# Kernel tuning notes

Hardware: AMD Instinct MI355X
Metric: run time of the kernel (lower is better)

The kernel has to match this reference:

```python
import jax, jax.numpy as jnp
import numpy as np
from jax import lax

B, C, H, W = 2, 3, 112, 112
PERCENTILE = 95.0


def setup_inputs() -> dict:
    key = jax.random.key(0)
    kx, ky = jax.random.split(key)
    x = jax.random.normal(kx, (B, C, H, W), dtype=jnp.float32)
    y = jax.random.randint(ky, (B, H, W), 0, C)
    return {"x": x, "y": y}


def _masked_quantile(vals, mask, q):
    # torch.quantile (linear interpolation) over entries of `vals` where mask is True.
    n = jnp.sum(mask)
    s = jnp.sort(jnp.where(mask, vals, jnp.inf))  # valid entries first, inf-padded
    pos = q * jnp.maximum(n - 1, 0).astype(vals.dtype)
    lo = jnp.floor(pos).astype(jnp.int32)
    hi = jnp.ceil(pos).astype(jnp.int32)
    frac = pos - lo.astype(vals.dtype)
    v = s[lo] * (1.0 - frac) + s[hi] * frac
    return jnp.where(n > 0, v, jnp.zeros((), vals.dtype))


def _forward(x, y):
    b, c = x.shape[0], x.shape[1]
    n = H * W
    pred = jnp.argmax(x, axis=1).reshape(b, n)   # [b, N] predicted labels
    gt = y.reshape(b, n).astype(pred.dtype)      # [b, N] gt labels

    # voxel coordinates of the full grid; nonzero() point sets become boolean masks over it
    ii, jj = jnp.meshgrid(jnp.arange(H, dtype=jnp.float32),
                          jnp.arange(W, dtype=jnp.float32), indexing="ij")
    coords = jnp.stack([ii.ravel(), jj.ravel()], axis=1)  # [N, 2]
    sq = jnp.sum(coords * coords, axis=1)
    d2 = sq[:, None] + sq[None, :] - 2.0 * (coords @ coords.T)
    D = jnp.sqrt(jnp.maximum(d2, 0.0))  # [N, N] symmetric all-pairs voxel distances

    cls = jnp.arange(c, dtype=pred.dtype)
    seg_masks = (pred[:, None, :] == cls[None, :, None]).reshape(b * c, n)  # [b*c, N]
    gt_masks = (gt[:, None, :] == cls[None, :, None]).reshape(b * c, n)
    q = jnp.float32(PERCENTILE / 100.0)

    def one(masks):
        seg_m, gt_m = masks
        # min distance from every voxel to the gt / seg point set
        d_to_gt = jnp.min(jnp.where(gt_m[None, :], D, jnp.inf), axis=1)   # [N]
        d_to_seg = jnp.min(jnp.where(seg_m[None, :], D, jnp.inf), axis=1)  # [N]
        hd1 = _masked_quantile(d_to_gt, seg_m, q)   # over seg points
        hd2 = _masked_quantile(d_to_seg, gt_m, q)   # over gt points
        hd = jnp.maximum(hd1, hd2)
        ok = (jnp.sum(seg_m) > 0) & (jnp.sum(gt_m) > 0)  # empty set -> 0.0
        return jnp.where(ok, hd, jnp.zeros((), D.dtype))

    hd_vals = lax.map(one, (seg_masks, gt_masks))  # sequential over b*c pairs, one [N,N] temp at a time
    return jnp.mean(hd_vals)


def reference(x, y):
    return _forward(x, y)
```

## Files before the change

### kernel.cpp

```cpp
#include <hip/hip_runtime.h>

#define BB 2
#define CC 3
#define HH 112
#define WW 112
#define NN (HH*WW)
#define NPAIR (BB*CC)
#define NCOMBO (NPAIR*2)
#define NBINS 24643
#define HWORDS ((NBINS+1)/2)
#define INF29 (1<<29)
#define RCH 8
#define NCHUNK (HH/RCH)
#define NTHR 1024
#define NFW (NN/64)
#define POISON 0xAAAAAAAAu
#define CSTRIDE 16
#define CTR_INTS ((NCOMBO+1)*CSTRIDE)

typedef unsigned long long ull;

__device__ __forceinline__ int predLab(const float* __restrict__ xb) {
    float v0 = xb[0], v1 = xb[NN], v2 = xb[2*(size_t)NN];
    int lab = 0; float best = v0;
    if (v1 > best) { best = v1; lab = 1; }
    if (v2 > best) lab = 2;
    return lab;
}

__device__ __forceinline__ void sinku(unsigned v) { asm volatile("" :: "v"(v)); }
__device__ __forceinline__ void sinkf(float v)    { asm volatile("" :: "v"(v)); }

union Smem {
    struct {
        ull flatW[NFW];
        unsigned colQ[4][WW];
        int G[RCH][WW];
    } ab;
    unsigned hist[HWORDS];
};

__global__ __launch_bounds__(NTHR) void fused_kernel(
        const float* __restrict__ x, const int* __restrict__ yl,
        unsigned* __restrict__ ghist, unsigned* __restrict__ ctrs,
        float* __restrict__ qvalg, int* __restrict__ qcntg,
        float* __restrict__ out) {
    __shared__ Smem sm;
    __shared__ int pscan[NTHR];
    __shared__ float vlh[2];
    __shared__ int lastFlag, gLastFlag;

    const int tid = threadIdx.x;
    const int m     = blockIdx.x / NCHUNK;
    const int chunk = blockIdx.x % NCHUNK;
    const int r0 = chunk * RCH;
    const int pair = m >> 1, src = m & 1;
    const int b = pair / CC, c = pair % CC;
    const float* xb = x + (size_t)b * CC * NN;
    const int*   yb = yl + b * NN;
    unsigned* ghm = ghist + m * HWORDS;
    unsigned* ctr = ctrs + m * CSTRIDE;

    const int lane = tid & 63, wid = tid >> 6;
    #pragma unroll
    for (int k = 0; k < (NN + NTHR - 1)/NTHR; k++) {
        int v = k*NTHR + tid;
        bool in = (v < NN);
        int lab = 0;
        if (in) lab = src ? predLab(xb + v) : yb[v];
        ull m64 = __ballot(in && lab == c);
        int w = k*(NTHR/64) + wid;
        if (lane == 0 && w < NFW) sm.ab.flatW[w] = m64;
    }
    __syncthreads();

    if (tid < 4*WW) {
        int xcolT = tid % WW, q = tid / WW;
        const unsigned* flatU = (const unsigned*)sm.ab.flatW;
        int jmax = (q == 3) ? (HH - 96) : 32;
        unsigned acc = 0;
        int p = (q*32)*WW + xcolT;
        for (int j = 0; j < jmax; j++) {
            acc |= ((flatU[p >> 5] >> (p & 31)) & 1u) << j;
            p += WW;
        }
        sm.ab.colQ[q][xcolT] = acc;
    }
    __syncthreads();

    const int xcol = tid % WW, rsel = tid / WW;
    const bool act = (tid < RCH*WW);

    if (act) {
        ull lo = sm.ab.colQ[0][xcol] | ((ull)sm.ab.colQ[1][xcol] << 32);
        ull hi = sm.ab.colQ[2][xcol] | ((ull)sm.ab.colQ[3][xcol] << 32);
        int r = r0 + rsel;
        ull mleLo, mleHi, mgeLo, mgeHi;
        if (r < 64) {
            mleLo = (2ull << r) - 1;  mleHi = 0;
            mgeLo = ~((1ull << r) - 1); mgeHi = ~0ull;
        } else {
            int rr = r - 64;
            mleLo = ~0ull; mleHi = (2ull << rr) - 1;
            mgeLo = 0;     mgeHi = ~((1ull << rr) - 1);
        }
        ull sL = lo & mleLo, sH = hi & mleHi;
        ull tL = lo & mgeLo, tH = hi & mgeHi;
        int posUp = sH ? (127 - (int)__builtin_clzll(sH))
                       : (sL ? (63 - (int)__builtin_clzll(sL)) : -4000);
        int posDn = tL ? (int)__builtin_ctzll(tL)
                       : (tH ? 64 + (int)__builtin_ctzll(tH) : 8000);
        int d = min(r - posUp, posDn - r);
        sm.ab.G[rsel][xcol] = d * d;
    }
    __syncthreads();

    int dreg = INF29;
    if (act) {
        int a0 = INF29, a1 = INF29, a2 = INF29, a3 = INF29;
        #pragma unroll 4
        for (int xx = 0; xx < WW; xx += 4) {
            int d0 = xcol-xx, d1 = xcol-xx-1, d2v = xcol-xx-2, d3 = xcol-xx-3;
            a0 = min(a0, d0*d0   + sm.ab.G[rsel][xx]);
            a1 = min(a1, d1*d1   + sm.ab.G[rsel][xx+1]);
            a2 = min(a2, d2v*d2v + sm.ab.G[rsel][xx+2]);
            a3 = min(a3, d3*d3   + sm.ab.G[rsel][xx+3]);
        }
        dreg = min(min(a0,a1), min(a2,a3));
    }
    __syncthreads();

    for (int i = tid; i < HWORDS; i += NTHR) sm.hist[i] = 0;
    __syncthreads();
    if (act) {
        int v = (r0 + rsel) * WW + xcol;
        int qlab = src ? yb[v] : predLab(xb + v);
        if (qlab == c) {
            int d2 = min(dreg, NBINS-1);
            atomicAdd(&sm.hist[d2 >> 1], 1u << ((d2 & 1) << 4));
        }
    }
    __syncthreads();

    for (int i = tid; i < HWORDS; i += NTHR) {
        unsigned w = sm.hist[i];
        if (w) {
            sinku(atomicCAS(&ghm[i], POISON, 0u));
            sinku(atomicAdd(&ghm[i], w));
        }
    }
    __syncthreads();

    if (tid == 0) {
        sinku(atomicCAS(ctr, POISON, 0u));
        unsigned prev = atomicAdd(ctr, 1u);
        lastFlag = (prev == NCHUNK - 1);
    }
    __syncthreads();
    if (!lastFlag) return;
    if (tid == 0) atomicExch(ctr, 0u);

    for (int i = tid; i < HWORDS; i += NTHR) {
        unsigned old = atomicExch(&ghm[i], 0u);
        if (old == POISON) old = 0u;
        sm.hist[i] = old;
    }
    __syncthreads();

    const int CHUNKB = (NBINS + NTHR - 1) / NTHR;
    int lo = tid * CHUNKB, hiE = min(lo + CHUNKB, NBINS);
    int s = 0;
    for (int i = lo; i < hiE; i++) s += (sm.hist[i >> 1] >> ((i & 1) << 4)) & 0xffff;
    pscan[tid] = s;
    __syncthreads();
    for (int off = 1; off < NTHR; off <<= 1) {
        int v = pscan[tid];
        int add = (tid >= off) ? pscan[tid - off] : 0;
        __syncthreads();
        pscan[tid] = v + add;
        __syncthreads();
    }
    int n = pscan[NTHR - 1];
    float qv = 0.f;
    if (n > 0) {
        float pos  = 0.95f * (float)(n - 1);
        int   klo  = (int)floorf(pos);
        int   khi  = (int)ceilf(pos);
        float frac = pos - (float)klo;
        int excl = pscan[tid] - s;
        for (int which = 0; which < 2; which++) {
            int r = which ? khi : klo;
            if (r >= excl && r < pscan[tid]) {
                int cacc = excl;
                for (int i = lo; i < hiE; i++) {
                    cacc += (sm.hist[i >> 1] >> ((i & 1) << 4)) & 0xffff;
                    if (cacc > r) { vlh[which] = sqrtf((float)i); break; }
                }
            }
            __syncthreads();
        }
        qv = vlh[0] * (1.f - frac) + vlh[1] * frac;
    }

    if (tid == 0) {
        sinkf(atomicExch(&qvalg[m], qv));
        sinku((unsigned)atomicExch(&qcntg[m], n));
    }
    __syncthreads();
    if (tid == 0) {
        unsigned* done = ctrs + NCOMBO * CSTRIDE;
        sinku(atomicCAS(done, POISON, 0u));
        unsigned prev = atomicAdd(done, 1u);
        gLastFlag = (prev == NCOMBO - 1);
    }
    __syncthreads();
    if (!gLastFlag) return;
    if (tid == 0) atomicExch(ctrs + NCOMBO * CSTRIDE, 0u);

    __shared__ float rq[NCOMBO];
    __shared__ int rc[NCOMBO];
    if (tid < NCOMBO) {
        rq[tid] = atomicAdd(&qvalg[tid], 0.f);
        rc[tid] = atomicAdd(&qcntg[tid], 0);
    }
    __syncthreads();
    if (tid == 0) {
        float ssum = 0.f;
        for (int p = 0; p < NPAIR; p++) {
            float hd = 0.f;
            if (rc[2*p] > 0 && rc[2*p+1] > 0)
                hd = fmaxf(rq[2*p], rq[2*p+1]);
            ssum += hd;
        }
        out[0] = ssum / (float)NPAIR;
    }
}

extern "C" void kernel_launch(void* const* d_in, const int* in_sizes, int n_in,
                              void* d_out, int out_size, void* d_ws, size_t ws_size,
                              hipStream_t stream) {
    const float* x = (const float*)d_in[0];
    const int*   y = (const int*)d_in[1];
    float* out = (float*)d_out;

    unsigned* ws    = (unsigned*)d_ws;
    unsigned* ctrs  = ws;
    unsigned* ghist = ctrs + CTR_INTS;
    float*    qvalg = (float*)(ghist + NCOMBO*HWORDS);
    int*      qcntg = (int*)(qvalg + NCOMBO);

    fused_kernel<<<NCOMBO*NCHUNK, NTHR, 0, stream>>>(x, y, ghist, ctrs,
                                                     qvalg, qcntg, out);
}
```

Baseline: 26.59 us.

## Halve row chunks, vectorize mask build, use shuffle scan and drop poison CAS

Uses 4-row chunks with 512-thread blocks, giving more, smaller blocks. The label mask is built with float4/int4 loads and shared atomicOr instead of per-element ballots. The block prefix scan now uses wave shuffles in place of a barrier-heavy Hillis-Steele loop. Per-word poison atomicCAS calls are replaced by a sentinel word subtraction, and the count array is folded into a -1 quantile marker. More blocks means the full-image mask work is repeated more often in total, and correctness now depends on the poison-initialised workspace convention.

```diff
diff --git a/kernel.cpp b/kernel.cpp
--- a/kernel.cpp
+++ b/kernel.cpp
@@ -9,46 +9,41 @@
 #define NCOMBO (NPAIR*2)
 #define NBINS 24643
 #define HWORDS ((NBINS+1)/2)
+#define HSTRIDE (HWORDS+16)
 #define INF29 (1<<29)
-#define RCH 8
+#define RCH 4
 #define NCHUNK (HH/RCH)
-#define NTHR 1024
-#define NFW (NN/64)
+#define NTHR 512
+#define NQ4 (NN/4)
+#define NFW2 (NN/32)
 #define POISON 0xAAAAAAAAu
 #define CSTRIDE 16
 #define CTR_INTS ((NCOMBO+1)*CSTRIDE)
 
 typedef unsigned long long ull;
 
-__device__ __forceinline__ int predLab(const float* __restrict__ xb) {
-    float v0 = xb[0], v1 = xb[NN], v2 = xb[2*(size_t)NN];
-    int lab = 0; float best = v0;
-    if (v1 > best) { best = v1; lab = 1; }
-    if (v2 > best) lab = 2;
+__device__ __forceinline__ int predLab3(float a, float b, float d) {
+    int lab = 0; float best = a;
+    if (b > best) { best = b; lab = 1; }
+    if (d > best) lab = 2;
     return lab;
 }
-
 __device__ __forceinline__ void sinku(unsigned v) { asm volatile("" :: "v"(v)); }
 __device__ __forceinline__ void sinkf(float v)    { asm volatile("" :: "v"(v)); }
-
-union Smem {
-    struct {
-        ull flatW[NFW];
-        unsigned colQ[4][WW];
-        int G[RCH][WW];
-    } ab;
-    unsigned hist[HWORDS];
-};
 
 __global__ __launch_bounds__(NTHR) void fused_kernel(
         const float* __restrict__ x, const int* __restrict__ yl,
         unsigned* __restrict__ ghist, unsigned* __restrict__ ctrs,
-        float* __restrict__ qvalg, int* __restrict__ qcntg,
-        float* __restrict__ out) {
-    __shared__ Smem sm;
-    __shared__ int pscan[NTHR];
+        float* __restrict__ qvalg, float* __restrict__ out) {
+    __shared__ unsigned flatU[NFW2];
+    __shared__ unsigned colQ[4][WW];
+    __shared__ int G[RCH][WW];
+    __shared__ unsigned hist[HWORDS];
+    __shared__ int wsum[NTHR/64];
     __shared__ float vlh[2];
     __shared__ int lastFlag, gLastFlag;
+    __shared__ unsigned pbase;
+    __shared__ float rq[NCOMBO];
 
     const int tid = threadIdx.x;
     const int m     = blockIdx.x / NCHUNK;
@@ -58,42 +53,57 @@
     const int b = pair / CC, c = pair % CC;
     const float* xb = x + (size_t)b * CC * NN;
     const int*   yb = yl + b * NN;
-    unsigned* ghm = ghist + m * HWORDS;
+    unsigned* ghm = ghist + m * HSTRIDE;
     unsigned* ctr = ctrs + m * CSTRIDE;
-
-    const int lane = tid & 63, wid = tid >> 6;
+    unsigned* done = ctrs + NCOMBO * CSTRIDE;
+
+    for (int i = tid; i < NFW2; i += NTHR) flatU[i] = 0u;
+    for (int i = tid; i < HWORDS; i += NTHR) hist[i] = 0u;
+    __syncthreads();
+
     #pragma unroll
-    for (int k = 0; k < (NN + NTHR - 1)/NTHR; k++) {
-        int v = k*NTHR + tid;
-        bool in = (v < NN);
-        int lab = 0;
-        if (in) lab = src ? predLab(xb + v) : yb[v];
-        ull m64 = __ballot(in && lab == c);
-        int w = k*(NTHR/64) + wid;
-        if (lane == 0 && w < NFW) sm.ab.flatW[w] = m64;
-    }
-    __syncthreads();
-
-    if (tid < 4*WW) {
+    for (int k = 0; k < (NQ4 + NTHR - 1) / NTHR; k++) {
+        int t4 = k * NTHR + tid;
+        if (t4 < NQ4) {
+            int v4 = t4 * 4;
+            unsigned nib;
+            if (src) {
+                const float4 a  = *(const float4*)(xb + v4);
+                const float4 b4 = *(const float4*)(xb + NN + v4);
+                const float4 d4 = *(const float4*)(xb + 2 * NN + v4);
+                nib  = (unsigned)(predLab3(a.x, b4.x, d4.x) == c);
+                nib |= (unsigned)(predLab3(a.y, b4.y, d4.y) == c) << 1;
+                nib |= (unsigned)(predLab3(a.z, b4.z, d4.z) == c) << 2;
+                nib |= (unsigned)(predLab3(a.w, b4.w, d4.w) == c) << 3;
+            } else {
+                const int4 yv = *(const int4*)(yb + v4);
+                nib  = (unsigned)(yv.x == c) | ((unsigned)(yv.y == c) << 1)
+                     | ((unsigned)(yv.z == c) << 2) | ((unsigned)(yv.w == c) << 3);
+            }
+            if (nib) atomicOr(&flatU[t4 >> 3], nib << ((t4 & 7) << 2));
+        }
+    }
+    __syncthreads();
+
+    if (tid < 4 * WW) {
         int xcolT = tid % WW, q = tid / WW;
-        const unsigned* flatU = (const unsigned*)sm.ab.flatW;
         int jmax = (q == 3) ? (HH - 96) : 32;
         unsigned acc = 0;
-        int p = (q*32)*WW + xcolT;
+        int p = (q * 32) * WW + xcolT;
         for (int j = 0; j < jmax; j++) {
             acc |= ((flatU[p >> 5] >> (p & 31)) & 1u) << j;
             p += WW;
         }
-        sm.ab.colQ[q][xcolT] = acc;
+        colQ[q][xcolT] = acc;
     }
     __syncthreads();
 
     const int xcol = tid % WW, rsel = tid / WW;
-    const bool act = (tid < RCH*WW);
+    const bool act = (tid < RCH * WW);
 
     if (act) {
-        ull lo = sm.ab.colQ[0][xcol] | ((ull)sm.ab.colQ[1][xcol] << 32);
-        ull hi = sm.ab.colQ[2][xcol] | ((ull)sm.ab.colQ[3][xcol] << 32);
+        ull lo64 = colQ[0][xcol] | ((ull)colQ[1][xcol] << 32);
+        ull hi64 = colQ[2][xcol] | ((ull)colQ[3][xcol] << 32);
         int r = r0 + rsel;
         ull mleLo, mleHi, mgeLo, mgeHi;
         if (r < 64) {
@@ -104,132 +114,125 @@
             mleLo = ~0ull; mleHi = (2ull << rr) - 1;
             mgeLo = 0;     mgeHi = ~((1ull << rr) - 1);
         }
-        ull sL = lo & mleLo, sH = hi & mleHi;
-        ull tL = lo & mgeLo, tH = hi & mgeHi;
+        ull sL = lo64 & mleLo, sH = hi64 & mleHi;
+        ull tL = lo64 & mgeLo, tH = hi64 & mgeHi;
         int posUp = sH ? (127 - (int)__builtin_clzll(sH))
                        : (sL ? (63 - (int)__builtin_clzll(sL)) : -4000);
         int posDn = tL ? (int)__builtin_ctzll(tL)
                        : (tH ? 64 + (int)__builtin_ctzll(tH) : 8000);
         int d = min(r - posUp, posDn - r);
-        sm.ab.G[rsel][xcol] = d * d;
-    }
-    __syncthreads();
-
-    int dreg = INF29;
+        G[rsel][xcol] = d * d;
+    }
+    __syncthreads();
+
     if (act) {
         int a0 = INF29, a1 = INF29, a2 = INF29, a3 = INF29;
         #pragma unroll 4
         for (int xx = 0; xx < WW; xx += 4) {
-            int d0 = xcol-xx, d1 = xcol-xx-1, d2v = xcol-xx-2, d3 = xcol-xx-3;
-            a0 = min(a0, d0*d0   + sm.ab.G[rsel][xx]);
-            a1 = min(a1, d1*d1   + sm.ab.G[rsel][xx+1]);
-            a2 = min(a2, d2v*d2v + sm.ab.G[rsel][xx+2]);
-            a3 = min(a3, d3*d3   + sm.ab.G[rsel][xx+3]);
-        }
-        dreg = min(min(a0,a1), min(a2,a3));
-    }
-    __syncthreads();
-
-    for (int i = tid; i < HWORDS; i += NTHR) sm.hist[i] = 0;
-    __syncthreads();
-    if (act) {
+            int d0 = xcol - xx, d1 = xcol - xx - 1, d2v = xcol - xx - 2, d3 = xcol - xx - 3;
+            a0 = min(a0, d0 * d0   + G[rsel][xx]);
+            a1 = min(a1, d1 * d1   + G[rsel][xx + 1]);
+            a2 = min(a2, d2v * d2v + G[rsel][xx + 2]);
+            a3 = min(a3, d3 * d3   + G[rsel][xx + 3]);
+        }
+        int dreg = min(min(a0, a1), min(a2, a3));
         int v = (r0 + rsel) * WW + xcol;
-        int qlab = src ? yb[v] : predLab(xb + v);
+        int qlab = src ? yb[v] : predLab3(xb[v], xb[NN + v], xb[2 * NN + v]);
         if (qlab == c) {
-            int d2 = min(dreg, NBINS-1);
-            atomicAdd(&sm.hist[d2 >> 1], 1u << ((d2 & 1) << 4));
+            int d2 = min(dreg, NBINS - 1);
+            atomicAdd(&hist[d2 >> 1], 1u << ((d2 & 1) << 4));
         }
     }
     __syncthreads();
 
     for (int i = tid; i < HWORDS; i += NTHR) {
-        unsigned w = sm.hist[i];
-        if (w) {
-            sinku(atomicCAS(&ghm[i], POISON, 0u));
-            sinku(atomicAdd(&ghm[i], w));
-        }
+        unsigned w = hist[i];
+        if (w) sinku(atomicAdd(&ghm[i], w));
     }
     __syncthreads();
 
     if (tid == 0) {
-        sinku(atomicCAS(ctr, POISON, 0u));
         unsigned prev = atomicAdd(ctr, 1u);
+        if (prev >= POISON) prev -= POISON;
         lastFlag = (prev == NCHUNK - 1);
     }
     __syncthreads();
     if (!lastFlag) return;
     if (tid == 0) atomicExch(ctr, 0u);
 
-    for (int i = tid; i < HWORDS; i += NTHR) {
-        unsigned old = atomicExch(&ghm[i], 0u);
-        if (old == POISON) old = 0u;
-        sm.hist[i] = old;
-    }
+    if (tid == 0) pbase = (atomicExch(&ghm[HWORDS], 0u) == POISON) ? POISON : 0u;
+    __syncthreads();
+    for (int i = tid; i < HWORDS; i += NTHR)
+        hist[i] = atomicExch(&ghm[i], 0u) - pbase;
     __syncthreads();
 
     const int CHUNKB = (NBINS + NTHR - 1) / NTHR;
     int lo = tid * CHUNKB, hiE = min(lo + CHUNKB, NBINS);
     int s = 0;
-    for (int i = lo; i < hiE; i++) s += (sm.hist[i >> 1] >> ((i & 1) << 4)) & 0xffff;
-    pscan[tid] = s;
-    __syncthreads();
-    for (int off = 1; off < NTHR; off <<= 1) {
-        int v = pscan[tid];
-        int add = (tid >= off) ? pscan[tid - off] : 0;
-        __syncthreads();
-        pscan[tid] = v + add;
-        __syncthreads();
-    }
-    int n = pscan[NTHR - 1];
+    for (int i = lo; i < hiE; i++) s += (hist[i >> 1] >> ((i & 1) << 4)) & 0xffff;
+
+    const int lane = tid & 63, wid = tid >> 6;
+    int incl = s;
+    #pragma unroll
+    for (int o = 1; o < 64; o <<= 1) {
+        int t2 = __shfl_up(incl, o, 64);
+        if (lane >= o) incl += t2;
+    }
+    if (lane == 63) wsum[wid] = incl;
+    __syncthreads();
+    if (wid == 0) {
+        int vv = (lane < NTHR / 64) ? wsum[lane] : 0;
+        #pragma unroll
+        for (int o = 1; o < NTHR / 64; o <<= 1) {
+            int t2 = __shfl_up(vv, o, 64);
+            if (lane >= o) vv += t2;
+        }
+        if (lane < NTHR / 64) wsum[lane] = vv;
+    }
+    __syncthreads();
+    incl += (wid > 0) ? wsum[wid - 1] : 0;
+    int excl = incl - s;
+    int n = wsum[NTHR / 64 - 1];
+
     float qv = 0.f;
     if (n > 0) {
         float pos  = 0.95f * (float)(n - 1);
         int   klo  = (int)floorf(pos);
         int   khi  = (int)ceilf(pos);
         float frac = pos - (float)klo;
-        int excl = pscan[tid] - s;
+        #pragma unroll
         for (int which = 0; which < 2; which++) {
             int r = which ? khi : klo;
-            if (r >= excl && r < pscan[tid]) {
+            if (r >= excl && r < incl) {
                 int cacc = excl;
                 for (int i = lo; i < hiE; i++) {
-                    cacc += (sm.hist[i >> 1] >> ((i & 1) << 4)) & 0xffff;
+                    cacc += (hist[i >> 1] >> ((i & 1) << 4)) & 0xffff;
                     if (cacc > r) { vlh[which] = sqrtf((float)i); break; }
                 }
             }
-            __syncthreads();
-        }
+        }
+        __syncthreads();
         qv = vlh[0] * (1.f - frac) + vlh[1] * frac;
     }
 
+    if (tid == 0) sinkf(atomicExch(&qvalg[m], (n > 0) ? qv : -1.0f));
+    __syncthreads();
     if (tid == 0) {
-        sinkf(atomicExch(&qvalg[m], qv));
-        sinku((unsigned)atomicExch(&qcntg[m], n));
-    }
-    __syncthreads();
-    if (tid == 0) {
-        unsigned* done = ctrs + NCOMBO * CSTRIDE;
-        sinku(atomicCAS(done, POISON, 0u));
         unsigned prev = atomicAdd(done, 1u);
+        if (prev >= POISON) prev -= POISON;
         gLastFlag = (prev == NCOMBO - 1);
     }
     __syncthreads();
     if (!gLastFlag) return;
-    if (tid == 0) atomicExch(ctrs + NCOMBO * CSTRIDE, 0u);
-
-    __shared__ float rq[NCOMBO];
-    __shared__ int rc[NCOMBO];
-    if (tid < NCOMBO) {
-        rq[tid] = atomicAdd(&qvalg[tid], 0.f);
-        rc[tid] = atomicAdd(&qcntg[tid], 0);
-    }
+    if (tid == 0) atomicExch(done, 0u);
+
+    if (tid < NCOMBO) rq[tid] = atomicAdd(&qvalg[tid], 0.f);
     __syncthreads();
     if (tid == 0) {
         float ssum = 0.f;
         for (int p = 0; p < NPAIR; p++) {
-            float hd = 0.f;
-            if (rc[2*p] > 0 && rc[2*p+1] > 0)
-                hd = fmaxf(rq[2*p], rq[2*p+1]);
+            float a = rq[2 * p], b2 = rq[2 * p + 1];
+            float hd = (a >= 0.f && b2 >= 0.f) ? fmaxf(a, b2) : 0.f;
             ssum += hd;
         }
         out[0] = ssum / (float)NPAIR;
@@ -246,9 +249,7 @@
     unsigned* ws    = (unsigned*)d_ws;
     unsigned* ctrs  = ws;
     unsigned* ghist = ctrs + CTR_INTS;
-    float*    qvalg = (float*)(ghist + NCOMBO*HWORDS);
-    int*      qcntg = (int*)(qvalg + NCOMBO);
-
-    fused_kernel<<<NCOMBO*NCHUNK, NTHR, 0, stream>>>(x, y, ghist, ctrs,
-                                                     qvalg, qcntg, out);
+    float*    qvalg = (float*)(ghist + NCOMBO*HSTRIDE);
+
+    fused_kernel<<<NCOMBO * NCHUNK, NTHR, 0, stream>>>(x, y, ghist, ctrs, qvalg, out);
 }
```

Result: slower. 28.76 us (+8.2%).
